# Optimization experiments

Hardware: AMD Instinct MI355X
Metric: run time of the kernel (lower is better)

The kernel has to match this reference:

```python
import jax, jax.numpy as jnp
import numpy as np

H = 16        # num_attention_heads
G = 16        # groups
SCALE_MIN = 0.95
SCALE_MAX = 1.05


def setup_inputs() -> dict:
    key = jax.random.key(0)
    ks = jax.random.split(key, 9)
    B, S, E = 2, 2048, 1024
    d = {
        'hidden_states': jax.random.normal(ks[0], (B, S, E), jnp.float32),
        'Wq': jax.random.normal(ks[1], (E, E), jnp.float32) * (E ** -0.5),
        'bq': jax.random.normal(ks[2], (E,), jnp.float32) * 0.02,
        'Wk': jax.random.normal(ks[3], (E, E), jnp.float32) * (E ** -0.5),
        'bk': jax.random.normal(ks[4], (E,), jnp.float32) * 0.02,
        'Wv': jax.random.normal(ks[5], (E, E), jnp.float32) * (E ** -0.5),
        'bv': jax.random.normal(ks[6], (E,), jnp.float32) * 0.02,
        'Ws': jax.random.normal(ks[7], (H * G, E), jnp.float32) * (E ** -0.5),
        'bs': jax.random.normal(ks[8], (H * G,), jnp.float32) * 0.02,
    }
    return d


def _shape_heads(x, B, S):
    # [B,S,h*D] -> [B,h,S,D]
    return x.reshape(B, S, H, -1).transpose(0, 2, 1, 3)


def reference(hidden_states, Wq, bq, Wk, bk, Wv, bv, Ws, bs):
    B, S, E = hidden_states.shape
    D = E // H            # head dim = 64
    gd = D // G           # group dim = 4

    Q = _shape_heads(hidden_states @ Wq.T + bq, B, S)   # [B,h,S,D]
    K = _shape_heads(hidden_states @ Wk.T + bk, B, S)
    V = _shape_heads(hidden_states @ Wv.T + bv, B, S)

    # groupwise dynamic scales, narrow sigmoid range
    s_logits = hidden_states @ Ws.T + bs                 # [B,S,h*g]
    s = jax.nn.sigmoid(s_logits) * (SCALE_MAX - SCALE_MIN) + SCALE_MIN
    s = s.reshape(B, S, H, G).transpose(0, 2, 1, 3)      # [B,h,S,g]
    s = jnp.repeat(s, gd, axis=-1)                       # [B,h,S,D]

    Q = Q * s  # apply_to='q'

    scores = jnp.einsum('bhsd,bhtd->bhst', Q, K) / jnp.sqrt(jnp.float32(D))
    probs = jax.nn.softmax(scores, axis=-1)
    ctx = jnp.einsum('bhst,bhtd->bhsd', probs, V)        # [B,h,S,D]
    ctx = ctx.transpose(0, 2, 1, 3).reshape(B, S, H * D)
    return ctx
```

## Files before the change

kernel.cpp:

```cpp
#include <hip/hip_runtime.h>

typedef short bf16x8 __attribute__((ext_vector_type(8)));
typedef float f32x4 __attribute__((ext_vector_type(4)));

__device__ inline float bf2f(ushort u) {
    unsigned v = ((unsigned)u) << 16;
    return __builtin_bit_cast(float, v);
}
__device__ inline ushort f2bf(float f) {
    unsigned u = __builtin_bit_cast(unsigned, f);
    u += 0x7fffu + ((u >> 16) & 1u);
    return (ushort)(u >> 16);
}
__device__ inline void async_load16(const ushort* g, ushort* l) {
    __builtin_amdgcn_global_load_lds((const __attribute__((address_space(1))) void*)g,
                                     (__attribute__((address_space(3))) void*)l, 16, 0, 0);
}

__global__ void cast_all(const float* __restrict__ hs, const float* __restrict__ Wq,
                         const float* __restrict__ Wk, const float* __restrict__ Wv,
                         const float* __restrict__ Ws,
                         ushort* __restrict__ dhs, ushort* __restrict__ dWq,
                         ushort* __restrict__ dWk, ushort* __restrict__ dWv,
                         ushort* __restrict__ dWs)
{
    int bid = blockIdx.x;
    const float* src; ushort* dst; int off;
    if (bid < 2048)      { src = hs; dst = dhs; off = bid; }
    else if (bid < 2560) { src = Wq; dst = dWq; off = bid - 2048; }
    else if (bid < 3072) { src = Wk; dst = dWk; off = bid - 2560; }
    else if (bid < 3584) { src = Wv; dst = dWv; off = bid - 3072; }
    else                 { src = Ws; dst = dWs; off = bid - 3584; }
    int i = (off * 256 + threadIdx.x) * 8;
    float4 a = *(const float4*)(src + i);
    float4 b = *(const float4*)(src + i + 4);
    union { ushort u[8]; float4 v; } o;
    o.u[0] = f2bf(a.x); o.u[1] = f2bf(a.y); o.u[2] = f2bf(a.z); o.u[3] = f2bf(a.w);
    o.u[4] = f2bf(b.x); o.u[5] = f2bf(b.y); o.u[6] = f2bf(b.z); o.u[7] = f2bf(b.w);
    *(float4*)(dst + i) = o.v;
}

__launch_bounds__(256, 4)
__global__ void fused_qkvs(const ushort* __restrict__ X,
                           const ushort* __restrict__ Wq, const ushort* __restrict__ Wk,
                           const ushort* __restrict__ Wv, const ushort* __restrict__ Ws,
                           const float* __restrict__ bq, const float* __restrict__ bk,
                           const float* __restrict__ bv, const float* __restrict__ bs,
                           ushort* __restrict__ Qb, ushort* __restrict__ Kb,
                           ushort* __restrict__ VtG, float* __restrict__ sb)
{
    __shared__ __align__(16) ushort Sm[128 * 136];
    ushort* As = Sm;
    ushort* Bs = Sm + 128 * 64;

    const int tid = threadIdx.x, w = tid >> 6, lane = tid & 63;
    const int l15 = lane & 15, quad = lane >> 4;
    const int lrow = lane >> 3;
    const int gchunk = ((lane & 7) ^ lrow) * 8;

    const int wid = blockIdx.x;
    const int r8 = wid & 7, jj = wid >> 3;
    const int by = (jj & 3) * 8 + r8;
    const int xb = jj >> 2;
    const int m0 = by * 128;

    const ushort* W; const float* bias; int n0, mode;
    if (xb < 8)       { W = Wq; bias = bq; n0 = xb * 128;        mode = 1; }
    else if (xb < 16) { W = Wk; bias = bk; n0 = (xb - 8) * 128;  mode = 0; }
    else if (xb < 24) { W = Wv; bias = bv; n0 = (xb - 16) * 128; mode = 2; }
    else              { W = Ws; bias = bs; n0 = (xb - 24) * 128; mode = 3; }

    const int wm = (w >> 1) * 64, wn = (w & 1) * 64;

    f32x4 acc[4][4];
    for (int i = 0; i < 4; i++) for (int j = 0; j < 4; j++) acc[i][j] = (f32x4){0.f, 0.f, 0.f, 0.f};

    for (int k0 = 0; k0 < 1024; k0 += 64) {
        __syncthreads();
        for (int c = 0; c < 4; ++c) {
            int r = w * 32 + c * 8;
            async_load16(&X[(size_t)(m0 + r + lrow) * 1024 + k0 + gchunk], &As[r * 64]);
            async_load16(&W[(size_t)(n0 + r + lrow) * 1024 + k0 + gchunk], &Bs[r * 64]);
        }
        __syncthreads();
        for (int kk = 0; kk < 64; kk += 32) {
            const int csw = quad + (kk >> 3);
            bf16x8 a[4], b[4];
            for (int i = 0; i < 4; i++)
                a[i] = *(const bf16x8*)&As[(wm + i * 16 + l15) * 64 + ((csw ^ (l15 & 7)) * 8)];
            for (int j = 0; j < 4; j++)
                b[j] = *(const bf16x8*)&Bs[(wn + j * 16 + l15) * 64 + ((csw ^ (l15 & 7)) * 8)];
            for (int i = 0; i < 4; i++)
                for (int j = 0; j < 4; j++)
                    acc[i][j] = __builtin_amdgcn_mfma_f32_16x16x32_bf16(a[i], b[j], acc[i][j], 0, 0, 0);
        }
    }

    const float QSCALE = 0.125f * 1.44269504f;

    if (mode == 3) {
        for (int i = 0; i < 4; i++)
            for (int j = 0; j < 4; j++) {
                int gn = n0 + wn + j * 16 + l15;
                float bv_ = bias[gn];
                for (int r = 0; r < 4; r++) {
                    int gm = m0 + wm + i * 16 + quad * 4 + r;
                    float v = acc[i][j][r] + bv_;
                    float sg = 1.0f / (1.0f + exp2f(-v * 1.44269504f));
                    sb[(size_t)gm * 256 + gn] = sg * 0.1f + 0.95f;
                }
            }
        return;
    }

    __syncthreads();

    if (mode == 2) {
        for (int i = 0; i < 4; i++)
            for (int j = 0; j < 4; j++) {
                int gnl = wn + j * 16 + l15;
                float bv_ = bias[n0 + gnl];
                ushort4 pk;
                pk.x = f2bf(acc[i][j][0] + bv_);
                pk.y = f2bf(acc[i][j][1] + bv_);
                pk.z = f2bf(acc[i][j][2] + bv_);
                pk.w = f2bf(acc[i][j][3] + bv_);
                *(ushort4*)&Sm[gnl * 136 + wm + i * 16 + quad * 4] = pk;
            }
        __syncthreads();
        const int bb = m0 >> 11, sloc = m0 & 2047;
        for (int it = 0; it < 8; ++it) {
            int d = (tid >> 4) + it * 16;
            int s8 = (tid & 15) * 8;
            float4 v = *(float4*)&Sm[d * 136 + s8];
            int h = (n0 + d) >> 6, dd = d & 63;
            *(float4*)&VtG[(size_t)(bb * 16 + h) * 131072 + (size_t)dd * 2048 + sloc + s8] = v;
        }
    } else {
        for (int i = 0; i < 4; i++)
            for (int j = 0; j < 4; j++) {
                int gnl = wn + j * 16 + l15;
                float bv_ = bias[n0 + gnl];
                for (int r = 0; r < 4; r++) {
                    float v = acc[i][j][r] + bv_;
                    if (mode == 1) v *= QSCALE;
                    Sm[(wm + i * 16 + quad * 4 + r) * 136 + gnl] = f2bf(v);
                }
            }
        __syncthreads();
        ushort* dst = (mode == 1) ? Qb : Kb;
        for (int it = 0; it < 8; ++it) {
            int row = (tid >> 4) + it * 16, c = (tid & 15) * 8;
            *(float4*)&dst[(size_t)(m0 + row) * 1024 + n0 + c] = *(float4*)&Sm[row * 136 + c];
        }
    }
}

__launch_bounds__(256, 2)
__global__ void attn_kernel(const ushort* __restrict__ Q, const ushort* __restrict__ K,
                            const ushort* __restrict__ Vt, const float* __restrict__ sb,
                            float* __restrict__ out)
{
    __shared__ __align__(16) ushort Qs[128 * 72];
    __shared__ __align__(16) ushort Ps[128 * 72];
    __shared__ __align__(16) ushort Ks0[64 * 64];
    __shared__ __align__(16) ushort Ks1[64 * 64];
    __shared__ __align__(16) ushort Vs0[64 * 64];
    __shared__ __align__(16) ushort Vs1[64 * 64];

    const int tid = threadIdx.x, w = tid >> 6, lane = tid & 63;
    const int l15 = lane & 15, quad = lane >> 4;
    const int lrow = lane >> 3;
    const int gchunk = ((lane & 7) ^ lrow) * 8;

    const int wid = blockIdx.x;
    const int r8 = wid & 7, jj = wid >> 3;
    const int bh = (jj & 3) * 8 + r8;
    const int qx = jj >> 2;
    const int b = bh >> 4, h = bh & 15;
    const int q0 = qx * 128;
    const size_t rowbase = (size_t)b * 2048;
    const int cbase = h * 64;

    for (int it = 0; it < 4; ++it) {
        int l = tid + it * 256;
        int r = l >> 3, c = (l & 7) * 8;
        union { float4 f; ushort u[8]; } uu, oo;
        uu.f = *(const float4*)&Q[(rowbase + q0 + r) * 1024 + cbase + c];
        const float* sp = &sb[(rowbase + q0 + r) * 256 + ((cbase + c) >> 2)];
        float s0 = sp[0], s1 = sp[1];
        for (int j = 0; j < 4; j++) oo.u[j] = f2bf(bf2f(uu.u[j]) * s0);
        for (int j = 4; j < 8; j++) oo.u[j] = f2bf(bf2f(uu.u[j]) * s1);
        *(float4*)&Qs[r * 72 + c] = oo.f;
    }

    for (int c = 0; c < 2; ++c) {
        int r = w * 16 + c * 8;
        async_load16(&K[(rowbase + r + lrow) * 1024 + cbase + gchunk], &Ks0[r * 64]);
        async_load16(&Vt[(size_t)bh * 131072 + (size_t)(r + lrow) * 2048 + gchunk], &Vs0[r * 64]);
    }
    __syncthreads();

    bf16x8 aq[2][2];
    for (int mt = 0; mt < 2; mt++)
        for (int kk2 = 0; kk2 < 2; kk2++)
            aq[mt][kk2] = *(const bf16x8*)&Qs[(w * 32 + mt * 16 + l15) * 72 + kk2 * 32 + quad * 8];

    ushort* pbase = &Ps[(w * 32 + quad * 4) * 72 + l15];

    float lsum[2][4];
    f32x4 o[2][4];
    for (int mt = 0; mt < 2; mt++) for (int r = 0; r < 4; r++) lsum[mt][r] = 0.f;
    for (int mt = 0; mt < 2; mt++) for (int nt = 0; nt < 4; nt++) o[mt][nt] = (f32x4){0.f, 0.f, 0.f, 0.f};

#define ATTN_STEP(KC, VC, KN, VN, KT, PREFETCH)                                                         \
    {                                                                                                   \
        __syncthreads();                       \
        if (PREFETCH) {                                                                                 \
            int nk = (KT) + 1;                                                                          \
            for (int c = 0; c < 2; ++c) {                                                               \
                int r = w * 16 + c * 8;                                                                 \
                async_load16(&K[(rowbase + nk * 64 + r + lrow) * 1024 + cbase + gchunk], &KN[r * 64]);  \
                async_load16(&Vt[(size_t)bh * 131072 + (size_t)(r + lrow) * 2048 + nk * 64 + gchunk],   \
                             &VN[r * 64]);                                                              \
            }                                                                                           \
        }                                                                                               \
        bf16x8 kb[2][4], vb[2][4];                                                                      \
        for (int kk2 = 0; kk2 < 2; kk2++)                                                               \
            for (int nt = 0; nt < 4; nt++) {                                                            \
                const int csw = (((quad + kk2 * 4)) ^ (l15 & 7)) * 8;                                   \
                kb[kk2][nt] = *(const bf16x8*)&KC[(nt * 16 + l15) * 64 + csw];                          \
                vb[kk2][nt] = *(const bf16x8*)&VC[(nt * 16 + l15) * 64 + csw];                          \
            }                                                                                           \
        f32x4 sacc[2][4];                                                                               \
        for (int mt = 0; mt < 2; mt++)                                                                  \
            for (int nt = 0; nt < 4; nt++) sacc[mt][nt] = (f32x4){0.f, 0.f, 0.f, 0.f};                  \
        for (int kk2 = 0; kk2 < 2; kk2++)                                                               \
            for (int mt = 0; mt < 2; mt++)                                                              \
                for (int nt = 0; nt < 4; nt++)                                                          \
                    sacc[mt][nt] = __builtin_amdgcn_mfma_f32_16x16x32_bf16(aq[mt][kk2], kb[kk2][nt],    \
                                                                           sacc[mt][nt], 0, 0, 0);      \
        for (int half = 0; half < 2; half++) {                                                          \
            for (int mt = 0; mt < 2; mt++)                                                              \
                for (int nt = 2 * half; nt < 2 * half + 2; nt++)                                        \
                    for (int r = 0; r < 4; r++) {                                                       \
                        float p = exp2f(sacc[mt][nt][r]);                                               \
                        lsum[mt][r] += p;                                                               \
                        unsigned u_ = __builtin_bit_cast(unsigned, p) + 0x8000u;                        \
                        pbase[mt * 1152 + r * 72 + nt * 16] = (ushort)(u_ >> 16);                       \
                    }                                                                                   \
            bf16x8 a_[2];                                                                               \
            for (int mt = 0; mt < 2; mt++)                                                              \
                a_[mt] = *(const bf16x8*)&Ps[(w * 32 + mt * 16 + l15) * 72 + half * 32 + quad * 8];     \
            for (int mt = 0; mt < 2; mt++)                                                              \
                for (int nt = 0; nt < 4; nt++)                                                          \
                    o[mt][nt] = __builtin_amdgcn_mfma_f32_16x16x32_bf16(a_[mt], vb[half][nt],           \
                                                                        o[mt][nt], 0, 0, 0);            \
        }                                                                                               \
    }

    for (int kt = 0; kt < 32; kt += 2) {
        ATTN_STEP(Ks0, Vs0, Ks1, Vs1, kt, 1);
        ATTN_STEP(Ks1, Vs1, Ks0, Vs0, kt + 1, (kt + 2 < 32));
    }
#undef ATTN_STEP

    for (int mt = 0; mt < 2; mt++)
        for (int r = 0; r < 4; r++) {
            float s = lsum[mt][r];
            for (int off = 1; off < 16; off <<= 1) s += __shfl_xor(s, off);
            lsum[mt][r] = s;
        }

    for (int mt = 0; mt < 2; mt++) {
        for (int r = 0; r < 4; r++) {
            float inv = 1.0f / lsum[mt][r];
            int q = q0 + w * 32 + mt * 16 + quad * 4 + r;
            size_t base = (rowbase + q) * 1024 + cbase;
            for (int nt = 0; nt < 4; nt++)
                out[base + nt * 16 + l15] = o[mt][nt][r] * inv;
        }
    }
}

extern "C" void kernel_launch(void* const* d_in, const int* in_sizes, int n_in,
                              void* d_out, int out_size, void* d_ws, size_t ws_size,
                              hipStream_t stream) {
    const float* hs = (const float*)d_in[0];
    const float* Wq = (const float*)d_in[1];
    const float* bq = (const float*)d_in[2];
    const float* Wk = (const float*)d_in[3];
    const float* bk = (const float*)d_in[4];
    const float* Wv = (const float*)d_in[5];
    const float* bv = (const float*)d_in[6];
    const float* Ws = (const float*)d_in[7];
    const float* bs = (const float*)d_in[8];
    float* outp = (float*)d_out;

    char* ws = (char*)d_ws;
    ushort* Qb    = (ushort*)(ws);
    ushort* Kb    = (ushort*)(ws + 8388608);
    ushort* VtG   = (ushort*)(ws + 16777216);
    float*  sb    = (float* )(ws + 25165824);
    ushort* hs_bf = (ushort*)(ws + 29360128);
    ushort* Wq_bf = (ushort*)(ws + 37748736);
    ushort* Wk_bf = (ushort*)(ws + 39845888);
    ushort* Wv_bf = (ushort*)(ws + 41943040);
    ushort* Ws_bf = (ushort*)(ws + 44040192);

    dim3 blk(256);
    cast_all<<<dim3(3712), blk, 0, stream>>>(hs, Wq, Wk, Wv, Ws,
                                             hs_bf, Wq_bf, Wk_bf, Wv_bf, Ws_bf);
    fused_qkvs<<<dim3(832), blk, 0, stream>>>(hs_bf, Wq_bf, Wk_bf, Wv_bf, Ws_bf,
                                              bq, bk, bv, bs, Qb, Kb, VtG, sb);
    attn_kernel<<<dim3(512), blk, 0, stream>>>(Qb, Kb, VtG, sb, outp);
}
```

Before: 189.5 us.

## Transpose QK^T MFMA, pack P stores, alias Q staging with K/V LDS for occupancy

Computes scores as K·Q^T so each lane holds four consecutive key columns for a single query row. P can then be packed into bf16 pairs with perm and written with one 8-byte swizzled store instead of scalar ushort stores. Row sums become a single per-lane scalar reduced with two shuffles. The Q staging buffer now aliases the K/V double buffers and P shrinks, which cuts LDS so launch bounds can target three blocks per SM. The risks are an extra barrier, register pressure at the higher occupancy, and a leftover dead pointer expression.

```diff
diff --git a/kernel.cpp b/kernel.cpp
--- a/kernel.cpp
+++ b/kernel.cpp
@@ -156,17 +156,18 @@
     }
 }
 
-__launch_bounds__(256, 2)
+__launch_bounds__(256, 3)
 __global__ void attn_kernel(const ushort* __restrict__ Q, const ushort* __restrict__ K,
                             const ushort* __restrict__ Vt, const float* __restrict__ sb,
                             float* __restrict__ out)
 {
-    __shared__ __align__(16) ushort Qs[128 * 72];
-    __shared__ __align__(16) ushort Ps[128 * 72];
-    __shared__ __align__(16) ushort Ks0[64 * 64];
-    __shared__ __align__(16) ushort Ks1[64 * 64];
-    __shared__ __align__(16) ushort Vs0[64 * 64];
-    __shared__ __align__(16) ushort Vs1[64 * 64];
+    __shared__ __align__(16) ushort SmA[4 * 64 * 64];
+    __shared__ __align__(16) ushort Ps[4 * 32 * 64];
+    ushort* Ks0 = SmA;
+    ushort* Ks1 = SmA + 4096;
+    ushort* Vs0 = SmA + 8192;
+    ushort* Vs1 = SmA + 12288;
+    ushort* Qs  = SmA;
 
     const int tid = threadIdx.x, w = tid >> 6, lane = tid & 63;
     const int l15 = lane & 15, quad = lane >> 4;
@@ -193,25 +194,28 @@
         for (int j = 4; j < 8; j++) oo.u[j] = f2bf(bf2f(uu.u[j]) * s1);
         *(float4*)&Qs[r * 72 + c] = oo.f;
     }
+    __syncthreads();
+
+    bf16x8 aq[2][2];
+    for (int mt = 0; mt < 2; mt++)
+        for (int kk2 = 0; kk2 < 2; kk2++)
+            aq[mt][kk2] = *(const bf16x8*)&Qs[(w * 32 + mt * 16 + l15) * 72 + kk2 * 32 + quad * 8];
+    __syncthreads();
 
     for (int c = 0; c < 2; ++c) {
         int r = w * 16 + c * 8;
         async_load16(&K[(rowbase + r + lrow) * 1024 + cbase + gchunk], &Ks0[r * 64]);
         async_load16(&Vt[(size_t)bh * 131072 + (size_t)(r + lrow) * 2048 + gchunk], &Vs0[r * 64]);
     }
-    __syncthreads();
-
-    bf16x8 aq[2][2];
-    for (int mt = 0; mt < 2; mt++)
-        for (int kk2 = 0; kk2 < 2; kk2++)
-            aq[mt][kk2] = *(const bf16x8*)&Qs[(w * 32 + mt * 16 + l15) * 72 + kk2 * 32 + quad * 8];
-
-    ushort* pbase = &Ps[(w * 32 + quad * 4) * 72 + l15];
-
-    float lsum[2][4];
+
+    ushort* pw = &Ps[w * 2048 + l15 * 64 + ((quad >> 1) ^ (l15 & 7) & 1 ? 0 : 0)]; (void)pw;
+    const int wrbase = w * 2048 + l15 * 64 + (quad & 1) * 4;
+    const int rdbase = w * 2048 + l15 * 64;
+
+    float lsum[2] = {0.f, 0.f};
     f32x4 o[2][4];
-    for (int mt = 0; mt < 2; mt++) for (int r = 0; r < 4; r++) lsum[mt][r] = 0.f;
     for (int mt = 0; mt < 2; mt++) for (int nt = 0; nt < 4; nt++) o[mt][nt] = (f32x4){0.f, 0.f, 0.f, 0.f};
+    const f32x4 z4 = (f32x4){0.f, 0.f, 0.f, 0.f};
 
 #define ATTN_STEP(KC, VC, KN, VN, KT, PREFETCH)                                                         \
     {                                                                                                   \
@@ -228,30 +232,39 @@
         bf16x8 kb[2][4], vb[2][4];                                                                      \
         for (int kk2 = 0; kk2 < 2; kk2++)                                                               \
             for (int nt = 0; nt < 4; nt++) {                                                            \
-                const int csw = (((quad + kk2 * 4)) ^ (l15 & 7)) * 8;                                   \
+                const int csw = ((quad + kk2 * 4) ^ (l15 & 7)) * 8;                                     \
                 kb[kk2][nt] = *(const bf16x8*)&KC[(nt * 16 + l15) * 64 + csw];                          \
                 vb[kk2][nt] = *(const bf16x8*)&VC[(nt * 16 + l15) * 64 + csw];                          \
             }                                                                                           \
-        f32x4 sacc[2][4];                                                                               \
+                              \
+        f32x4 st[2][4];                                                                                 \
         for (int mt = 0; mt < 2; mt++)                                                                  \
-            for (int nt = 0; nt < 4; nt++) sacc[mt][nt] = (f32x4){0.f, 0.f, 0.f, 0.f};                  \
-        for (int kk2 = 0; kk2 < 2; kk2++)                                                               \
-            for (int mt = 0; mt < 2; mt++)                                                              \
-                for (int nt = 0; nt < 4; nt++)                                                          \
-                    sacc[mt][nt] = __builtin_amdgcn_mfma_f32_16x16x32_bf16(aq[mt][kk2], kb[kk2][nt],    \
-                                                                           sacc[mt][nt], 0, 0, 0);      \
+            for (int kt2 = 0; kt2 < 4; kt2++) {                                                         \
+                st[mt][kt2] = __builtin_amdgcn_mfma_f32_16x16x32_bf16(kb[0][kt2], aq[mt][0], z4, 0, 0, 0); \
+                st[mt][kt2] = __builtin_amdgcn_mfma_f32_16x16x32_bf16(kb[1][kt2], aq[mt][1],            \
+                                                                      st[mt][kt2], 0, 0, 0);            \
+            }                                                                                           \
+        for (int mt = 0; mt < 2; mt++)                                                                  \
+            for (int kt2 = 0; kt2 < 4; kt2++) {                                                         \
+                float p0 = exp2f(st[mt][kt2][0]);                                                       \
+                float p1 = exp2f(st[mt][kt2][1]);                                                       \
+                float p2 = exp2f(st[mt][kt2][2]);                                                       \
+                float p3 = exp2f(st[mt][kt2][3]);                                                       \
+                lsum[mt] += (p0 + p1) + (p2 + p3);                                                      \
+                unsigned d0 = __builtin_amdgcn_perm(__builtin_bit_cast(unsigned, p1) + 0x8000u,         \
+                                                    __builtin_bit_cast(unsigned, p0) + 0x8000u,         \
+                                                    0x07060302u);                                       \
+                unsigned d1 = __builtin_amdgcn_perm(__builtin_bit_cast(unsigned, p3) + 0x8000u,         \
+                                                    __builtin_bit_cast(unsigned, p2) + 0x8000u,         \
+                                                    0x07060302u);                                       \
+                uint2 pk; pk.x = d0; pk.y = d1;                                                         \
+                *(uint2*)&Ps[wrbase + mt * 1024 + (((kt2 * 2 + (quad >> 1)) ^ (l15 & 7)) * 8)] = pk;    \
+            }                                                                                           \
+                                     \
         for (int half = 0; half < 2; half++) {                                                          \
-            for (int mt = 0; mt < 2; mt++)                                                              \
-                for (int nt = 2 * half; nt < 2 * half + 2; nt++)                                        \
-                    for (int r = 0; r < 4; r++) {                                                       \
-                        float p = exp2f(sacc[mt][nt][r]);                                               \
-                        lsum[mt][r] += p;                                                               \
-                        unsigned u_ = __builtin_bit_cast(unsigned, p) + 0x8000u;                        \
-                        pbase[mt * 1152 + r * 72 + nt * 16] = (ushort)(u_ >> 16);                       \
-                    }                                                                                   \
             bf16x8 a_[2];                                                                               \
             for (int mt = 0; mt < 2; mt++)                                                              \
-                a_[mt] = *(const bf16x8*)&Ps[(w * 32 + mt * 16 + l15) * 72 + half * 32 + quad * 8];     \
+                a_[mt] = *(const bf16x8*)&Ps[rdbase + mt * 1024 + (((half * 4 + quad) ^ (l15 & 7)) * 8)];\
             for (int mt = 0; mt < 2; mt++)                                                              \
                 for (int nt = 0; nt < 4; nt++)                                                          \
                     o[mt][nt] = __builtin_amdgcn_mfma_f32_16x16x32_bf16(a_[mt], vb[half][nt],           \
@@ -265,20 +278,21 @@
     }
 #undef ATTN_STEP
 
-    for (int mt = 0; mt < 2; mt++)
-        for (int r = 0; r < 4; r++) {
-            float s = lsum[mt][r];
-            for (int off = 1; off < 16; off <<= 1) s += __shfl_xor(s, off);
-            lsum[mt][r] = s;
-        }
+    float inv[2];
+    for (int mt = 0; mt < 2; mt++) {
+        float s = lsum[mt];
+        s += __shfl_xor(s, 16);
+        s += __shfl_xor(s, 32);
+        inv[mt] = 1.0f / s;
+    }
 
     for (int mt = 0; mt < 2; mt++) {
         for (int r = 0; r < 4; r++) {
-            float inv = 1.0f / lsum[mt][r];
+            float iv = __shfl(inv[mt], quad * 4 + r);
             int q = q0 + w * 32 + mt * 16 + quad * 4 + r;
             size_t base = (rowbase + q) * 1024 + cbase;
             for (int nt = 0; nt < 4; nt++)
-                out[base + nt * 16 + l15] = o[mt][nt][r] * inv;
+                out[base + nt * 16 + l15] = o[mt][nt][r] * iv;
         }
     }
 }
```

Result: no change. 186.3 us (-1.7%).
